# Kernel tuning notes

Measured on AMD Instinct MI355X. Metric: run time of the kernel, lower is better.

## Reference

```python
import jax, jax.numpy as jnp
import numpy as np

EPS = 1e-8


def setup_inputs() -> dict:
    key = jax.random.key(0)
    k1, k2, k3, k4 = jax.random.split(key, 4)
    B, Cin, Cout, K, S, H, W = 8, 512, 512, 3, 512, 64, 64
    return {
        "x": jax.random.normal(k1, (B, Cin, H, W), dtype=jnp.float32),
        "style": jax.random.normal(k2, (B, S), dtype=jnp.float32),
        "weight": jax.random.normal(k3, (1, Cout, Cin, K, K), dtype=jnp.float32),
        "mod_w": jax.random.normal(k4, (Cin, S), dtype=jnp.float32),
        "mod_b": jnp.ones((Cin,), dtype=jnp.float32),
    }


def reference(x, style, weight, mod_w, mod_b):
    B, Cin, H, W = x.shape
    Cout, K = weight.shape[1], weight.shape[-1]
    style_dim = mod_w.shape[1]
    conv_scale = 1.0 / np.sqrt(Cin * K * K)  # 1/sqrt(fan_in)
    mod_scale = 1.0 / np.sqrt(style_dim)     # EqualLinear scale (lr_mul=1)

    # EqualLinear modulation: (B, Cin)
    s = style @ (mod_w * mod_scale).T + mod_b

    # per-sample modulated weights: (B, Cout, Cin, K, K)
    w = conv_scale * weight * s[:, None, :, None, None]
    demod = jax.lax.rsqrt(jnp.sum(w * w, axis=(2, 3, 4)) + EPS)  # (B, Cout)
    w = w * demod[:, :, None, None, None]

    # grouped conv with groups = batch
    w = w.reshape(B * Cout, Cin, K, K)
    xg = x.reshape(1, B * Cin, H, W)
    pad = (K - 1) // 2
    out = jax.lax.conv_general_dilated(
        xg, w,
        window_strides=(1, 1),
        padding=[(pad, pad), (pad, pad)],
        dimension_numbers=("NCHW", "OIHW", "NCHW"),
        feature_group_count=B,
    )
    return out.reshape(B, Cout, out.shape[2], out.shape[3])
```

## Files before the change

kernel.cpp:

```cpp
#include <hip/hip_runtime.h>
#include <hip/hip_bf16.h>
#include <cstdint>
#include <cstddef>

typedef __bf16 bf16x8 __attribute__((ext_vector_type(8)));
typedef float f32x4 __attribute__((ext_vector_type(4)));
typedef unsigned int uintx4 __attribute__((ext_vector_type(4)));

#define CONV_SCALE 0.014731391274719738f
#define MOD_SCALE  0.044194173824159216f

__device__ __forceinline__ unsigned short f2bf(float v) {
  unsigned int u = __float_as_uint(v);
  return (unsigned short)((u + 0x7FFFu + ((u >> 16) & 1u)) >> 16);
}

__device__ __forceinline__ void gload16(const void* g, void* l) {
  __builtin_amdgcn_global_load_lds(
      (const __attribute__((address_space(1))) unsigned int*)g,
      (__attribute__((address_space(3))) unsigned int*)l, 16, 0, 0);
}

__global__ void k_modulate(const float* __restrict__ style,
                           const float* __restrict__ mod_w,
                           const float* __restrict__ mod_b,
                           float* __restrict__ s) {
  int blk = blockIdx.x;
  int b = blk >> 2, ch = blk & 3;
  int t = threadIdx.x;
  int ci = ch * 128 + (t >> 1), half = t & 1;
  const float* st = style + b * 512 + half * 256;
  const float* mw = mod_w + (size_t)ci * 512 + half * 256;
  float acc = 0.f;
  #pragma unroll 8
  for (int k = 0; k < 256; k += 4) {
    f32x4 a = *(const f32x4*)(st + k);
    f32x4 m = *(const f32x4*)(mw + k);
    acc += a[0] * m[0] + a[1] * m[1] + a[2] * m[2] + a[3] * m[3];
  }
  acc += __shfl_xor(acc, 1);
  if (half == 0) s[b * 512 + ci] = acc * MOD_SCALE + mod_b[ci];
}

__global__ void k_wTq(const float* __restrict__ weight,
                      unsigned short* __restrict__ wT,
                      float* __restrict__ wsq) {
  __shared__ float lds[4608];
  int co = blockIdx.x;
  int t = threadIdx.x;
  const float* w = weight + (size_t)co * 4608;
  #pragma unroll
  for (int i = 0; i < 18; ++i) lds[t + i * 256] = w[t + i * 256];
  __syncthreads();
  for (int i = t; i < 576; i += 256) {
    int tap = i / 64, c8 = (i & 63) * 8;
    union { uintx4 v; unsigned short us[8]; } pk;
    #pragma unroll
    for (int j = 0; j < 8; ++j) pk.us[j] = f2bf(lds[(c8 + j) * 9 + tap]);
    *(uintx4*)(wT + ((size_t)tap * 512 + co) * 512 + c8) = pk.v;
  }
  for (int ci = t; ci < 512; ci += 256) {
    float a = 0.f;
    #pragma unroll
    for (int tap = 0; tap < 9; ++tap) { float v = lds[ci * 9 + tap]; a += v * v; }
    wsq[co * 512 + ci] = a * (CONV_SCALE * CONV_SCALE);
  }
}

__global__ void k_demod(const float* __restrict__ wsq, const float* __restrict__ s,
                        float* __restrict__ demod) {
  int b = blockIdx.x;
  int co = threadIdx.x;
  const float* wq = wsq + (size_t)co * 512;
  const float* sb = s + b * 512;
  float acc = 0.f;
  #pragma unroll 4
  for (int ci = 0; ci < 512; ci += 4) {
    f32x4 q = *(const f32x4*)(wq + ci);
    f32x4 v = *(const f32x4*)(sb + ci);
    acc += q[0] * v[0] * v[0] + q[1] * v[1] * v[1] + q[2] * v[2] * v[2] + q[3] * v[3] * v[3];
  }
  demod[b * 512 + co] = rsqrtf(acc + 1e-8f);
}

__global__ void k_xT(const float* __restrict__ x, const float* __restrict__ s,
                     unsigned short* __restrict__ xT) {
  __shared__ float lds[128][68];
  int cc = blockIdx.x;
  int h = blockIdx.y;
  int b = blockIdx.z;
  int t = threadIdx.x;
  int w4 = (t & 15) * 4, rr = t >> 4;
  #pragma unroll
  for (int i = 0; i < 8; ++i) {
    int ci = i * 16 + rr;
    *(f32x4*)&lds[ci][w4] =
        *(const f32x4*)&x[(((size_t)(b * 512 + cc * 128 + ci)) * 64 + h) * 64 + w4];
  }
  __syncthreads();
  int pos = t >> 2, c4 = t & 3;
  #pragma unroll
  for (int q = 0; q < 4; ++q) {
    int cb = q * 32 + c4 * 8;
    union { uintx4 v; unsigned short us[8]; } pk;
    #pragma unroll
    for (int j = 0; j < 8; ++j) {
      int ci = cb + j;
      pk.us[j] = f2bf(lds[ci][pos] * s[b * 512 + cc * 128 + ci]);
    }
    *(uintx4*)(xT + (((size_t)(b * 64 + h)) * 64 + pos) * 512 + cc * 128 + cb) = pk.v;
  }
}

__global__ __launch_bounds__(256, 2) void k_conv(
    const unsigned short* __restrict__ xT,
    const unsigned short* __restrict__ wT,
    const float* __restrict__ demod,
    float* __restrict__ out) {
  __shared__ __align__(16) char lds_raw[62208];
  char* xlds = lds_raw;
  char* wlds = lds_raw + 25344;

  const int co_t = blockIdx.x;
  const int h_t  = blockIdx.y;
  const int b    = blockIdx.z;
  const int t = threadIdx.x;
  const int lane = t & 63, wv = t >> 6;
  const int h0 = h_t * 4;
  const int co0 = co_t * 64;
  const int l15 = lane & 15, kg = lane >> 4;

  {
    uintx4 z = {0u, 0u, 0u, 0u};
    for (int i = t; i < 1584; i += 256) ((uintx4*)xlds)[i] = z;
  }

  f32x4 acc[4][4] = {};

  for (int cc = 0; cc < 16; ++cc) {
    __syncthreads();
    for (int j = wv; j < 24; j += 4) {
      int r = j >> 2, k = j & 3;
      int hh = h0 - 1 + r;
      if ((unsigned)hh < 64u) {
        int p = r * 66 + 1 + k * 16 + (lane >> 2);
        const unsigned short* g = xT + (((size_t)(b * 64 + hh)) * 64 + k * 16 + (lane >> 2)) * 512
                                  + cc * 32 + (((lane & 3) ^ ((p >> 1) & 3)) << 3);
        gload16(g, xlds + (r * 66 + 1 + k * 16) * 64);
      }
    }
    for (int j = wv; j < 36; j += 4) {
      int row0 = j * 16;
      int row = row0 + (lane >> 2);
      int tap = row >> 6, co = row & 63;
      const unsigned short* g = wT + ((size_t)tap * 512 + co0 + co) * 512
                                + cc * 32 + (((lane & 3) ^ ((row >> 1) & 3)) << 3);
      gload16(g, wlds + row0 * 64);
    }
    __syncthreads();

    #pragma unroll
    for (int tap = 0; tap < 9; ++tap) {
      const int dh = tap / 3, dw = tap % 3;
      bf16x8 af[4], bfr[4];
      #pragma unroll
      for (int m = 0; m < 4; ++m) {
        int row = tap * 64 + m * 16 + l15;
        af[m] = *(const bf16x8*)(wlds + row * 64 + ((kg ^ ((row >> 1) & 3)) << 4));
      }
      #pragma unroll
      for (int n = 0; n < 4; ++n) {
        int p = (wv + dh) * 66 + n * 16 + l15 + dw;
        bfr[n] = *(const bf16x8*)(xlds + p * 64 + ((kg ^ ((p >> 1) & 3)) << 4));
      }
      #pragma unroll
      for (int m = 0; m < 4; ++m)
        #pragma unroll
        for (int n = 0; n < 4; ++n)
          acc[m][n] = __builtin_amdgcn_mfma_f32_16x16x32_bf16(af[m], bfr[n], acc[m][n], 0, 0, 0);
    }
  }

  const int h_out = h0 + wv;
  #pragma unroll
  for (int m = 0; m < 4; ++m) {
    #pragma unroll
    for (int r = 0; r < 4; ++r) {
      int co = co0 + m * 16 + kg * 4 + r;
      float scl = CONV_SCALE * demod[b * 512 + co];
      #pragma unroll
      for (int n = 0; n < 4; ++n) {
        out[(((size_t)(b * 512 + co)) * 64 + h_out) * 64 + n * 16 + l15] = acc[m][n][r] * scl;
      }
    }
  }
}

extern "C" void kernel_launch(void* const* d_in, const int* in_sizes, int n_in,
                              void* d_out, int out_size, void* d_ws, size_t ws_size,
                              hipStream_t stream) {
  const float* x      = (const float*)d_in[0];
  const float* style  = (const float*)d_in[1];
  const float* weight = (const float*)d_in[2];
  const float* mod_w  = (const float*)d_in[3];
  const float* mod_b  = (const float*)d_in[4];
  float* out = (float*)d_out;

  char* ws = (char*)d_ws;
  unsigned short* xT = (unsigned short*)ws;
  unsigned short* wT = (unsigned short*)(ws + 33554432);
  float* s     = (float*)(ws + 38273024);
  float* wsq   = (float*)(ws + 38289408);
  float* demod = (float*)(ws + 39337984);

  hipLaunchKernelGGL(k_modulate, dim3(32),       dim3(256), 0, stream, style, mod_w, mod_b, s);
  hipLaunchKernelGGL(k_wTq,      dim3(512),      dim3(256), 0, stream, weight, wT, wsq);
  hipLaunchKernelGGL(k_demod,    dim3(8),        dim3(512), 0, stream, wsq, s, demod);
  hipLaunchKernelGGL(k_xT,       dim3(4, 64, 8), dim3(256), 0, stream, x, s, xT);
  hipLaunchKernelGGL(k_conv,     dim3(8, 16, 8), dim3(256), 0, stream, xT, wT, demod, out);
}
```

Baseline: 201.5 us.

## Double conv output rows per block so each wave reuses weight fragments

The conv block tile grows from 4 to 8 output rows, and each wave now computes two rows. Each weight fragment loaded from LDS therefore feeds twice as many MFMAs. This also halves how often weight tiles are staged from global memory per output, and the grid shrinks to half as many blocks. In exchange, the accumulator register footprint doubles and LDS use rises to about 79 KB of dynamic shared memory, which needs a one-time attribute call and may limit occupancy.

```diff
diff --git a/kernel.cpp b/kernel.cpp
--- a/kernel.cpp
+++ b/kernel.cpp
@@ -117,36 +117,37 @@
     const unsigned short* __restrict__ wT,
     const float* __restrict__ demod,
     float* __restrict__ out) {
-  __shared__ __align__(16) char lds_raw[62208];
+  extern __shared__ __align__(16) char lds_raw[];
   char* xlds = lds_raw;
-  char* wlds = lds_raw + 25344;
+  char* wlds = lds_raw + 42240;
 
   const int co_t = blockIdx.x;
   const int h_t  = blockIdx.y;
   const int b    = blockIdx.z;
   const int t = threadIdx.x;
   const int lane = t & 63, wv = t >> 6;
-  const int h0 = h_t * 4;
+  const int h0 = h_t * 8;
   const int co0 = co_t * 64;
   const int l15 = lane & 15, kg = lane >> 4;
 
   {
     uintx4 z = {0u, 0u, 0u, 0u};
-    for (int i = t; i < 1584; i += 256) ((uintx4*)xlds)[i] = z;
-  }
-
-  f32x4 acc[4][4] = {};
+    for (int i = t; i < 2640; i += 256) ((uintx4*)xlds)[i] = z;
+  }
+
+  f32x4 acc[4][2][4] = {};
 
   for (int cc = 0; cc < 16; ++cc) {
     __syncthreads();
-    for (int j = wv; j < 24; j += 4) {
+    for (int j = wv; j < 40; j += 4) {
       int r = j >> 2, k = j & 3;
       int hh = h0 - 1 + r;
       if ((unsigned)hh < 64u) {
-        int p = r * 66 + 1 + k * 16 + (lane >> 2);
+        int p0 = r * 66 + 1 + k * 16;
+        int p = p0 + (lane >> 2);
         const unsigned short* g = xT + (((size_t)(b * 64 + hh)) * 64 + k * 16 + (lane >> 2)) * 512
                                   + cc * 32 + (((lane & 3) ^ ((p >> 1) & 3)) << 3);
-        gload16(g, xlds + (r * 66 + 1 + k * 16) * 64);
+        gload16(g, xlds + p0 * 64);
       }
     }
     for (int j = wv; j < 36; j += 4) {
@@ -162,35 +163,42 @@
     #pragma unroll
     for (int tap = 0; tap < 9; ++tap) {
       const int dh = tap / 3, dw = tap % 3;
-      bf16x8 af[4], bfr[4];
+      bf16x8 af[4], bfr[2][4];
       #pragma unroll
       for (int m = 0; m < 4; ++m) {
         int row = tap * 64 + m * 16 + l15;
         af[m] = *(const bf16x8*)(wlds + row * 64 + ((kg ^ ((row >> 1) & 3)) << 4));
       }
       #pragma unroll
-      for (int n = 0; n < 4; ++n) {
-        int p = (wv + dh) * 66 + n * 16 + l15 + dw;
-        bfr[n] = *(const bf16x8*)(xlds + p * 64 + ((kg ^ ((p >> 1) & 3)) << 4));
-      }
+      for (int r = 0; r < 2; ++r)
+        #pragma unroll
+        for (int n = 0; n < 4; ++n) {
+          int p = (2 * wv + r + dh) * 66 + n * 16 + l15 + dw;
+          bfr[r][n] = *(const bf16x8*)(xlds + p * 64 + ((kg ^ ((p >> 1) & 3)) << 4));
+        }
       #pragma unroll
       for (int m = 0; m < 4; ++m)
         #pragma unroll
-        for (int n = 0; n < 4; ++n)
-          acc[m][n] = __builtin_amdgcn_mfma_f32_16x16x32_bf16(af[m], bfr[n], acc[m][n], 0, 0, 0);
-    }
-  }
-
-  const int h_out = h0 + wv;
+        for (int r = 0; r < 2; ++r)
+          #pragma unroll
+          for (int n = 0; n < 4; ++n)
+            acc[m][r][n] = __builtin_amdgcn_mfma_f32_16x16x32_bf16(af[m], bfr[r][n], acc[m][r][n], 0, 0, 0);
+    }
+  }
+
   #pragma unroll
   for (int m = 0; m < 4; ++m) {
     #pragma unroll
-    for (int r = 0; r < 4; ++r) {
-      int co = co0 + m * 16 + kg * 4 + r;
+    for (int q = 0; q < 4; ++q) {
+      int co = co0 + m * 16 + kg * 4 + q;
       float scl = CONV_SCALE * demod[b * 512 + co];
       #pragma unroll
-      for (int n = 0; n < 4; ++n) {
-        out[(((size_t)(b * 512 + co)) * 64 + h_out) * 64 + n * 16 + l15] = acc[m][n][r] * scl;
+      for (int r = 0; r < 2; ++r) {
+        int h_out = h0 + 2 * wv + r;
+        #pragma unroll
+        for (int n = 0; n < 4; ++n) {
+          out[(((size_t)(b * 512 + co)) * 64 + h_out) * 64 + n * 16 + l15] = acc[m][r][n][q] * scl;
+        }
       }
     }
   }
@@ -213,9 +221,16 @@
   float* wsq   = (float*)(ws + 38289408);
   float* demod = (float*)(ws + 39337984);
 
+  static int lds_set = 0;
+  if (!lds_set) {
+    (void)hipFuncSetAttribute((const void*)k_conv,
+                              hipFuncAttributeMaxDynamicSharedMemorySize, 79104);
+    lds_set = 1;
+  }
+
   hipLaunchKernelGGL(k_modulate, dim3(32),       dim3(256), 0, stream, style, mod_w, mod_b, s);
   hipLaunchKernelGGL(k_wTq,      dim3(512),      dim3(256), 0, stream, weight, wT, wsq);
   hipLaunchKernelGGL(k_demod,    dim3(8),        dim3(512), 0, stream, wsq, s, demod);
   hipLaunchKernelGGL(k_xT,       dim3(4, 64, 8), dim3(256), 0, stream, x, s, xT);
-  hipLaunchKernelGGL(k_conv,     dim3(8, 16, 8), dim3(256), 0, stream, xT, wT, demod, out);
-}
+  hipLaunchKernelGGL(k_conv,     dim3(8, 8, 8),  dim3(256), 79104, stream, xT, wT, demod, out);
+}
```

Measured after the change: 193.9 us. 1.04x faster.
